# Optimization experiments

Measured on AMD Instinct MI355X. Metric: run time of the kernel, lower is better.

## Reference

```python
import jax, jax.numpy as jnp
import numpy as np

WINDOW = 21
PATCH = 1
H_PARAM = 0.1
EPS = 1e-10


def _box_sum(x, w):
    # Sum over a w x w sliding window (VALID), per (batch, channel).
    return jax.lax.reduce_window(x, 0.0, jax.lax.add,
                                 (1, 1, w, w), (1, 1, 1, 1), 'VALID')


def setup_inputs() -> dict:
    key = jax.random.key(0)
    noisy = jax.random.uniform(key, (8, 3, 512, 512), dtype=jnp.float32)
    return {"noisy": noisy}


def reference(noisy) -> jnp.ndarray:
    # Faithful vectorization of the per-pixel loop for patch_size=1.
    # For each pixel p=(i,j):
    #   window = padded[i:i+W, j:j+W]; center = noisy[i,j]
    #   dists  = mean((window - center)^2)
    #   weights = exp(-dists / h^2)            # shape (B, C)
    #   patch  = window[0, 0] = padded[i, j]   # top-left of window (half_patch=0)
    #   out[:, c, i, j] = sum_b weights[b,c] * patch[b,c]   (sum over BATCH)
    #   wsum[:, c, i, j] = sum_b weights[b,c]
    # out = clamp(out / (wsum + 1e-10), 0, 1)
    h2 = H_PARAM * H_PARAM
    W = WINDOW
    pad = W // 2
    B, C, Hh, Ww = noisy.shape
    padded = jnp.pad(noisy, ((0, 0), (0, 0), (pad, pad), (pad, pad)), mode='reflect')

    # mean((window - center)^2) = (S2 - 2*center*S1 + W^2*center^2) / W^2
    s1 = _box_sum(padded, W)                  # (B, C, H, W)
    s2 = _box_sum(padded * padded, W)
    n_win = jnp.asarray(W * W, dtype=noisy.dtype)
    dists = (s2 - 2.0 * noisy * s1 + n_win * noisy * noisy) / n_win

    weights = jnp.exp(-dists / h2)            # (B, C, H, W)
    patch = padded[:, :, :Hh, :Ww]            # top-left pixel of each window

    num = jnp.sum(weights * patch, axis=0, keepdims=True)   # (1, C, H, W)
    den = jnp.sum(weights, axis=0, keepdims=True)
    out = num / (den + EPS)
    out = jnp.broadcast_to(out, noisy.shape)  # loop assigns same row to all b
    return jnp.clip(out, 0.0, 1.0)
```

## Files before the change

### kernel.cpp

```cpp
#include <hip/hip_runtime.h>

#define B 8
#define CCH 3
#define HH 512
#define WW 512
#define WIN 21
#define PAD 10
#define TSX 32
#define TSY 32
#define PTY 52
#define TROW 60
#define HSH 53
#define NSLOT 676

__global__ __launch_bounds__(256, 3) void nlm_fused_kernel(const float* __restrict__ noisy,
                                                           float* __restrict__ out) {
    __shared__ float  tile[PTY][TROW];
    __shared__ float2 hs_t[TSX][HSH];

    const int tid = threadIdx.x;
    const int x0 = blockIdx.x * TSX;
    const int y0 = blockIdx.y * TSY;
    const int ch = blockIdx.z;

    int   rowbase[3], gxs[3];
    float* ldsp[3];
    bool  valid[3], edge[3];
    #pragma unroll
    for (int k = 0; k < 3; ++k) {
        int s = tid + 256 * k;
        valid[k] = (s < NSLOT);
        int ss = valid[k] ? s : 0;
        int r  = ss / 13;
        int c4 = ss - r * 13;
        int gy = y0 + r - PAD;
        gy = (gy < 0) ? -gy : ((gy >= HH) ? (2 * (HH - 1) - gy) : gy);
        int gx = x0 + (c4 << 2) - PAD;
        rowbase[k] = gy * WW;
        gxs[k]     = gx;
        edge[k]    = (gx < 0) || (gx > WW - 4);
        ldsp[k]    = &tile[r][c4 << 2];
    }

    const float* src0 = noisy + (size_t)ch * (HH * WW);
    float4 pre[3];
    #pragma unroll
    for (int k = 0; k < 3; ++k) {
        if (valid[k]) {
            if (!edge[k]) {
                pre[k] = *(const float4*)(src0 + rowbase[k] + gxs[k]);
            } else {
                float tmp[4];
                #pragma unroll
                for (int t = 0; t < 4; ++t) {
                    int gx = gxs[k] + t;
                    gx = (gx < 0) ? -gx : ((gx >= WW) ? (2 * (WW - 1) - gx) : gx);
                    tmp[t] = src0[rowbase[k] + gx];
                }
                pre[k] = make_float4(tmp[0], tmp[1], tmp[2], tmp[3]);
            }
        }
    }

    float num[4] = {0.f, 0.f, 0.f, 0.f};
    float den[4] = {0.f, 0.f, 0.f, 0.f};

    const int tx  = tid & 31;
    const int ty0 = (tid >> 5) << 2;

    for (int b = 0; b < B; ++b) {
        __syncthreads();
        #pragma unroll
        for (int k = 0; k < 3; ++k)
            if (valid[k]) *(float4*)ldsp[k] = pre[k];
        __syncthreads();

        if (b < B - 1) {
            const float* srcn = noisy + (size_t)((b + 1) * CCH + ch) * (HH * WW);
            #pragma unroll
            for (int k = 0; k < 3; ++k) {
                if (valid[k]) {
                    if (!edge[k]) {
                        pre[k] = *(const float4*)(srcn + rowbase[k] + gxs[k]);
                    } else {
                        float tmp[4];
                        #pragma unroll
                        for (int t = 0; t < 4; ++t) {
                            int gx = gxs[k] + t;
                            gx = (gx < 0) ? -gx : ((gx >= WW) ? (2 * (WW - 1) - gx) : gx);
                            tmp[t] = srcn[rowbase[k] + gx];
                        }
                        pre[k] = make_float4(tmp[0], tmp[1], tmp[2], tmp[3]);
                    }
                }
            }
        }

        if (tid < PTY * 4) {
            int r   = tid >> 2;
            int cx0 = (tid & 3) << 3;
            float v[28];
            #pragma unroll
            for (int q = 0; q < 7; ++q)
                *(float4*)&v[q * 4] = *(const float4*)&tile[r][cx0 + (q << 2)];
            float s1 = 0.f, s2 = 0.f;
            #pragma unroll
            for (int k = 0; k <= 20; ++k) { s1 += v[k]; s2 = fmaf(v[k], v[k], s2); }
            hs_t[cx0][r] = make_float2(s1, s2);
            #pragma unroll
            for (int j = 1; j < 8; ++j) {
                float vo = v[j - 1], vn = v[j + 20];
                s1 += vn - vo;
                s2 += vn * vn - vo * vo;
                hs_t[cx0 + j][r] = make_float2(s1, s2);
            }
        }
        __syncthreads();

        float2 h0 = hs_t[tx][ty0];
        float2 h1 = hs_t[tx][ty0 + 1];
        float2 h2 = hs_t[tx][ty0 + 2];
        float vs1 = h0.x + h1.x + h2.x;
        float vs2 = h0.y + h1.y + h2.y;
        #pragma unroll
        for (int k = 3; k <= 20; ++k) {
            float2 h = hs_t[tx][ty0 + k];
            vs1 += h.x;
            vs2 += h.y;
        }
        const float kE = (-100.0f / 441.0f) * 1.44269504088896f;
        {
            float a = tile[ty0 + PAD][tx + PAD];
            float p = tile[ty0][tx];
            float dd = fmaf(a, fmaf(441.f, a, -2.f * vs1), vs2);
            float w = exp2f(dd * kE);
            num[0] += w * p; den[0] += w;
        }
        #pragma unroll
        for (int i = 1; i < 4; ++i) {
            float2 hn = hs_t[tx][ty0 + 20 + i];
            float2 ho = (i == 1) ? h0 : ((i == 2) ? h1 : h2);
            vs1 += hn.x - ho.x;
            vs2 += hn.y - ho.y;
            float a = tile[ty0 + i + PAD][tx + PAD];
            float p = tile[ty0 + i][tx];
            float dd = fmaf(a, fmaf(441.f, a, -2.f * vs1), vs2);
            float w = exp2f(dd * kE);
            num[i] += w * p; den[i] += w;
        }
    }

    #pragma unroll
    for (int i = 0; i < 4; ++i) {
        int y = y0 + ty0 + i;
        int x = x0 + tx;
        float v = num[i] / (den[i] + 1e-10f);
        v = v < 0.f ? 0.f : (v > 1.f ? 1.f : v);
        #pragma unroll
        for (int b = 0; b < B; ++b)
            out[((size_t)(b * CCH + ch) * HH + y) * WW + x] = v;
    }
}

extern "C" void kernel_launch(void* const* d_in, const int* in_sizes, int n_in,
                              void* d_out, int out_size, void* d_ws, size_t ws_size,
                              hipStream_t stream) {
    const float* noisy = (const float*)d_in[0];
    float* out = (float*)d_out;
    dim3 grid(WW / TSX, HH / TSY, CCH);
    nlm_fused_kernel<<<grid, dim3(256), 0, stream>>>(noisy, out);
}
```

Baseline: 88.96 us.

## Drop shared input tile; load horizontal sums directly from global with double-buffered LDS

Removes the shared-memory input tile and its staging stores. Each horizontal-sum thread now reads its 32-wide row segment straight from global memory, and each output thread loads its center and patch pixels directly. The horizontal-sum buffer is double-buffered, so each batch iteration needs only one barrier instead of three. The cost is more redundant global/L2 traffic, since overlapping halo reads are no longer shared and the register prefetch of the next batch is gone, which could expose load latency.

```diff
diff --git a/kernel.cpp b/kernel.cpp
--- a/kernel.cpp
+++ b/kernel.cpp
@@ -4,161 +4,124 @@
 #define CCH 3
 #define HH 512
 #define WW 512
+#define HW (HH * WW)
 #define WIN 21
 #define PAD 10
 #define TSX 32
 #define TSY 32
-#define PTY 52
-#define TROW 60
+#define ROWS 52
 #define HSH 53
-#define NSLOT 676
 
 __global__ __launch_bounds__(256, 3) void nlm_fused_kernel(const float* __restrict__ noisy,
                                                            float* __restrict__ out) {
-    __shared__ float  tile[PTY][TROW];
-    __shared__ float2 hs_t[TSX][HSH];
+    __shared__ float2 hs[2][TSX][HSH];
 
     const int tid = threadIdx.x;
     const int x0 = blockIdx.x * TSX;
     const int y0 = blockIdx.y * TSY;
     const int ch = blockIdx.z;
 
-    int   rowbase[3], gxs[3];
-    float* ldsp[3];
-    bool  valid[3], edge[3];
+    const int hr   = tid >> 2;
+    const int hsg  = tid & 3;
+    const bool hact = (tid < ROWS * 4);
+    int gy = y0 + hr - PAD;
+    gy = (gy < 0) ? -gy : ((gy >= HH) ? (2 * (HH - 1) - gy) : gy);
+    const int hrow = gy * WW;
+    const int xb   = x0 + (hsg << 3) - 12;
+    const bool hedge = (xb < 0) || (xb + 31 > WW - 1);
+
+    const int tx  = tid & 31;
+    const int ty0 = (tid >> 5) << 2;
+    int aoff[4], poff[4];
+    int pc = x0 + tx - PAD;
+    pc = (pc < 0) ? -pc : pc;
     #pragma unroll
-    for (int k = 0; k < 3; ++k) {
-        int s = tid + 256 * k;
-        valid[k] = (s < NSLOT);
-        int ss = valid[k] ? s : 0;
-        int r  = ss / 13;
-        int c4 = ss - r * 13;
-        int gy = y0 + r - PAD;
-        gy = (gy < 0) ? -gy : ((gy >= HH) ? (2 * (HH - 1) - gy) : gy);
-        int gx = x0 + (c4 << 2) - PAD;
-        rowbase[k] = gy * WW;
-        gxs[k]     = gx;
-        edge[k]    = (gx < 0) || (gx > WW - 4);
-        ldsp[k]    = &tile[r][c4 << 2];
-    }
-
-    const float* src0 = noisy + (size_t)ch * (HH * WW);
-    float4 pre[3];
-    #pragma unroll
-    for (int k = 0; k < 3; ++k) {
-        if (valid[k]) {
-            if (!edge[k]) {
-                pre[k] = *(const float4*)(src0 + rowbase[k] + gxs[k]);
-            } else {
-                float tmp[4];
-                #pragma unroll
-                for (int t = 0; t < 4; ++t) {
-                    int gx = gxs[k] + t;
-                    gx = (gx < 0) ? -gx : ((gx >= WW) ? (2 * (WW - 1) - gx) : gx);
-                    tmp[t] = src0[rowbase[k] + gx];
-                }
-                pre[k] = make_float4(tmp[0], tmp[1], tmp[2], tmp[3]);
-            }
-        }
+    for (int i = 0; i < 4; ++i) {
+        const int ay = y0 + ty0 + i;
+        aoff[i] = ay * WW + (x0 + tx);
+        int py = ay - PAD;
+        py = (py < 0) ? -py : py;
+        poff[i] = py * WW + pc;
     }
 
     float num[4] = {0.f, 0.f, 0.f, 0.f};
     float den[4] = {0.f, 0.f, 0.f, 0.f};
+    const float kE = (-100.0f / 441.0f) * 1.44269504088896f;
 
-    const int tx  = tid & 31;
-    const int ty0 = (tid >> 5) << 2;
+    int cur = 0;
+    for (int b = 0; b < B; ++b) {
+        const float* src = noisy + (size_t)(b * CCH + ch) * HW;
 
-    for (int b = 0; b < B; ++b) {
-        __syncthreads();
+        float a[4], p[4];
         #pragma unroll
-        for (int k = 0; k < 3; ++k)
-            if (valid[k]) *(float4*)ldsp[k] = pre[k];
-        __syncthreads();
+        for (int i = 0; i < 4; ++i) { a[i] = src[aoff[i]]; p[i] = src[poff[i]]; }
 
-        if (b < B - 1) {
-            const float* srcn = noisy + (size_t)((b + 1) * CCH + ch) * (HH * WW);
-            #pragma unroll
-            for (int k = 0; k < 3; ++k) {
-                if (valid[k]) {
-                    if (!edge[k]) {
-                        pre[k] = *(const float4*)(srcn + rowbase[k] + gxs[k]);
-                    } else {
-                        float tmp[4];
-                        #pragma unroll
-                        for (int t = 0; t < 4; ++t) {
-                            int gx = gxs[k] + t;
-                            gx = (gx < 0) ? -gx : ((gx >= WW) ? (2 * (WW - 1) - gx) : gx);
-                            tmp[t] = srcn[rowbase[k] + gx];
-                        }
-                        pre[k] = make_float4(tmp[0], tmp[1], tmp[2], tmp[3]);
-                    }
+        if (hact) {
+            float w[32];
+            if (!hedge) {
+                #pragma unroll
+                for (int q = 0; q < 8; ++q)
+                    *(float4*)&w[q * 4] = *(const float4*)(src + hrow + xb + (q << 2));
+            } else {
+                #pragma unroll
+                for (int m = 0; m < 28; ++m) {
+                    int gx = xb + 2 + m;
+                    gx = (gx < 0) ? -gx : ((gx >= WW) ? (2 * (WW - 1) - gx) : gx);
+                    w[m + 2] = src[hrow + gx];
                 }
             }
-        }
-
-        if (tid < PTY * 4) {
-            int r   = tid >> 2;
-            int cx0 = (tid & 3) << 3;
-            float v[28];
-            #pragma unroll
-            for (int q = 0; q < 7; ++q)
-                *(float4*)&v[q * 4] = *(const float4*)&tile[r][cx0 + (q << 2)];
             float s1 = 0.f, s2 = 0.f;
             #pragma unroll
-            for (int k = 0; k <= 20; ++k) { s1 += v[k]; s2 = fmaf(v[k], v[k], s2); }
-            hs_t[cx0][r] = make_float2(s1, s2);
+            for (int k = 0; k < 21; ++k) { s1 += w[k + 2]; s2 = fmaf(w[k + 2], w[k + 2], s2); }
+            const int c0 = hsg << 3;
+            hs[cur][c0][hr] = make_float2(s1, s2);
             #pragma unroll
             for (int j = 1; j < 8; ++j) {
-                float vo = v[j - 1], vn = v[j + 20];
+                float vo = w[j + 1], vn = w[j + 22];
                 s1 += vn - vo;
                 s2 += vn * vn - vo * vo;
-                hs_t[cx0 + j][r] = make_float2(s1, s2);
+                hs[cur][c0 + j][hr] = make_float2(s1, s2);
             }
         }
         __syncthreads();
 
-        float2 h0 = hs_t[tx][ty0];
-        float2 h1 = hs_t[tx][ty0 + 1];
-        float2 h2 = hs_t[tx][ty0 + 2];
+        const float2* col = &hs[cur][tx][0];
+        float2 h0 = col[ty0], h1 = col[ty0 + 1], h2 = col[ty0 + 2];
         float vs1 = h0.x + h1.x + h2.x;
         float vs2 = h0.y + h1.y + h2.y;
         #pragma unroll
         for (int k = 3; k <= 20; ++k) {
-            float2 h = hs_t[tx][ty0 + k];
+            float2 h = col[ty0 + k];
             vs1 += h.x;
             vs2 += h.y;
         }
-        const float kE = (-100.0f / 441.0f) * 1.44269504088896f;
         {
-            float a = tile[ty0 + PAD][tx + PAD];
-            float p = tile[ty0][tx];
-            float dd = fmaf(a, fmaf(441.f, a, -2.f * vs1), vs2);
-            float w = exp2f(dd * kE);
-            num[0] += w * p; den[0] += w;
+            float dd = fmaf(a[0], fmaf(441.f, a[0], -2.f * vs1), vs2);
+            float wgt = exp2f(dd * kE);
+            num[0] = fmaf(wgt, p[0], num[0]); den[0] += wgt;
         }
         #pragma unroll
         for (int i = 1; i < 4; ++i) {
-            float2 hn = hs_t[tx][ty0 + 20 + i];
+            float2 hn = col[ty0 + 20 + i];
             float2 ho = (i == 1) ? h0 : ((i == 2) ? h1 : h2);
             vs1 += hn.x - ho.x;
             vs2 += hn.y - ho.y;
-            float a = tile[ty0 + i + PAD][tx + PAD];
-            float p = tile[ty0 + i][tx];
-            float dd = fmaf(a, fmaf(441.f, a, -2.f * vs1), vs2);
-            float w = exp2f(dd * kE);
-            num[i] += w * p; den[i] += w;
+            float dd = fmaf(a[i], fmaf(441.f, a[i], -2.f * vs1), vs2);
+            float wgt = exp2f(dd * kE);
+            num[i] = fmaf(wgt, p[i], num[i]); den[i] += wgt;
         }
+        cur ^= 1;
     }
 
     #pragma unroll
     for (int i = 0; i < 4; ++i) {
-        int y = y0 + ty0 + i;
-        int x = x0 + tx;
+        const int y = y0 + ty0 + i;
+        const int x = x0 + tx;
         float v = num[i] / (den[i] + 1e-10f);
         v = v < 0.f ? 0.f : (v > 1.f ? 1.f : v);
         #pragma unroll
-        for (int b = 0; b < B; ++b)
-            out[((size_t)(b * CCH + ch) * HH + y) * WW + x] = v;
+        for (int bb = 0; bb < B; ++bb)
+            out[((size_t)(bb * CCH + ch) * HH + y) * WW + x] = v;
     }
 }
 
```

Result: slower. 138.2 us (+55.4%).

## Halve tile height to 16 rows and double-buffer the LDS tile

Applied to the files above, without the earlier changes.

Shrinks each block to a 32x16 output tile with 128 threads, doubling the grid to give more blocks for latency hiding, at the cost of a larger halo fraction (36 loaded rows for 16 output rows instead of 52 for 32). The shared tile becomes double-buffered so one of the two per-batch barriers can be dropped. Each thread now does up to two horizontal-sum tasks. The extra halo means more redundant global loads and horizontal-sum work per output pixel.

```diff
diff --git a/kernel.cpp b/kernel.cpp
--- a/kernel.cpp
+++ b/kernel.cpp
@@ -7,15 +7,17 @@
 #define WIN 21
 #define PAD 10
 #define TSX 32
-#define TSY 32
-#define PTY 52
+#define TSY 16
+#define PTY 36
 #define TROW 60
-#define HSH 53
-#define NSLOT 676
+#define HSH 37
+#define NSLOT 468
+#define NTHR 128
+#define HTASK (PTY * 4)
 
-__global__ __launch_bounds__(256, 3) void nlm_fused_kernel(const float* __restrict__ noisy,
-                                                           float* __restrict__ out) {
-    __shared__ float  tile[PTY][TROW];
+__global__ __launch_bounds__(NTHR, 3) void nlm_fused_kernel(const float* __restrict__ noisy,
+                                                            float* __restrict__ out) {
+    __shared__ float  tile[2][PTY][TROW];
     __shared__ float2 hs_t[TSX][HSH];
 
     const int tid = threadIdx.x;
@@ -23,12 +25,12 @@
     const int y0 = blockIdx.y * TSY;
     const int ch = blockIdx.z;
 
-    int   rowbase[3], gxs[3];
-    float* ldsp[3];
-    bool  valid[3], edge[3];
+    int   rowbase[4], gxs[4];
+    float* ldsp[4];
+    bool  valid[4], edge[4];
     #pragma unroll
-    for (int k = 0; k < 3; ++k) {
-        int s = tid + 256 * k;
+    for (int k = 0; k < 4; ++k) {
+        int s = tid + NTHR * k;
         valid[k] = (s < NSLOT);
         int ss = valid[k] ? s : 0;
         int r  = ss / 13;
@@ -39,13 +41,13 @@
         rowbase[k] = gy * WW;
         gxs[k]     = gx;
         edge[k]    = (gx < 0) || (gx > WW - 4);
-        ldsp[k]    = &tile[r][c4 << 2];
+        ldsp[k]    = &tile[0][r][c4 << 2];
     }
 
     const float* src0 = noisy + (size_t)ch * (HH * WW);
-    float4 pre[3];
+    float4 pre[4];
     #pragma unroll
-    for (int k = 0; k < 3; ++k) {
+    for (int k = 0; k < 4; ++k) {
         if (valid[k]) {
             if (!edge[k]) {
                 pre[k] = *(const float4*)(src0 + rowbase[k] + gxs[k]);
@@ -67,18 +69,19 @@
 
     const int tx  = tid & 31;
     const int ty0 = (tid >> 5) << 2;
+    const float kE = (-100.0f / 441.0f) * 1.44269504088896f;
 
+    int par = 0;
     for (int b = 0; b < B; ++b) {
-        __syncthreads();
         #pragma unroll
-        for (int k = 0; k < 3; ++k)
-            if (valid[k]) *(float4*)ldsp[k] = pre[k];
+        for (int k = 0; k < 4; ++k)
+            if (valid[k]) *(float4*)(ldsp[k] + par * (PTY * TROW)) = pre[k];
         __syncthreads();
 
         if (b < B - 1) {
             const float* srcn = noisy + (size_t)((b + 1) * CCH + ch) * (HH * WW);
             #pragma unroll
-            for (int k = 0; k < 3; ++k) {
+            for (int k = 0; k < 4; ++k) {
                 if (valid[k]) {
                     if (!edge[k]) {
                         pre[k] = *(const float4*)(srcn + rowbase[k] + gxs[k]);
@@ -96,13 +99,13 @@
             }
         }
 
-        if (tid < PTY * 4) {
-            int r   = tid >> 2;
-            int cx0 = (tid & 3) << 3;
+        auto hwork = [&](int t) {
+            int r   = t >> 2;
+            int cx0 = (t & 3) << 3;
             float v[28];
             #pragma unroll
             for (int q = 0; q < 7; ++q)
-                *(float4*)&v[q * 4] = *(const float4*)&tile[r][cx0 + (q << 2)];
+                *(float4*)&v[q * 4] = *(const float4*)&tile[par][r][cx0 + (q << 2)];
             float s1 = 0.f, s2 = 0.f;
             #pragma unroll
             for (int k = 0; k <= 20; ++k) { s1 += v[k]; s2 = fmaf(v[k], v[k], s2); }
@@ -114,7 +117,9 @@
                 s2 += vn * vn - vo * vo;
                 hs_t[cx0 + j][r] = make_float2(s1, s2);
             }
-        }
+        };
+        hwork(tid);
+        if (tid < HTASK - NTHR) hwork(tid + NTHR);
         __syncthreads();
 
         float2 h0 = hs_t[tx][ty0];
@@ -128,10 +133,9 @@
             vs1 += h.x;
             vs2 += h.y;
         }
-        const float kE = (-100.0f / 441.0f) * 1.44269504088896f;
         {
-            float a = tile[ty0 + PAD][tx + PAD];
-            float p = tile[ty0][tx];
+            float a = tile[par][ty0 + PAD][tx + PAD];
+            float p = tile[par][ty0][tx];
             float dd = fmaf(a, fmaf(441.f, a, -2.f * vs1), vs2);
             float w = exp2f(dd * kE);
             num[0] += w * p; den[0] += w;
@@ -142,12 +146,13 @@
             float2 ho = (i == 1) ? h0 : ((i == 2) ? h1 : h2);
             vs1 += hn.x - ho.x;
             vs2 += hn.y - ho.y;
-            float a = tile[ty0 + i + PAD][tx + PAD];
-            float p = tile[ty0 + i][tx];
+            float a = tile[par][ty0 + i + PAD][tx + PAD];
+            float p = tile[par][ty0 + i][tx];
             float dd = fmaf(a, fmaf(441.f, a, -2.f * vs1), vs2);
             float w = exp2f(dd * kE);
             num[i] += w * p; den[i] += w;
         }
+        par ^= 1;
     }
 
     #pragma unroll
@@ -157,8 +162,8 @@
         float v = num[i] / (den[i] + 1e-10f);
         v = v < 0.f ? 0.f : (v > 1.f ? 1.f : v);
         #pragma unroll
-        for (int b = 0; b < B; ++b)
-            out[((size_t)(b * CCH + ch) * HH + y) * WW + x] = v;
+        for (int bb = 0; bb < B; ++bb)
+            out[((size_t)(bb * CCH + ch) * HH + y) * WW + x] = v;
     }
 }
 
@@ -168,5 +173,5 @@
     const float* noisy = (const float*)d_in[0];
     float* out = (float*)d_out;
     dim3 grid(WW / TSX, HH / TSY, CCH);
-    nlm_fused_kernel<<<grid, dim3(256), 0, stream>>>(noisy, out);
+    nlm_fused_kernel<<<grid, dim3(NTHR), 0, stream>>>(noisy, out);
 }
```

Result: slower. 99.40 us (+11.7%).

## Double-buffer LDS tiles and use a lightweight LDS-only barrier

Applied to the files above, without the earlier changes.

The shared tile and horizontal-sum buffers are duplicated and alternate by batch parity. This removes the leading __syncthreads that kept the next batch's store from racing with reads of the previous one. The remaining barriers become an inline s_waitcnt lgkmcnt(0) plus s_barrier. That barrier does not wait on outstanding global loads, so the prefetch of the next batch can stay in flight across it. The cost is roughly double the LDS per block, which at 3 blocks per CU sits close to the per-CU LDS limit and could reduce occupancy.

```diff
diff --git a/kernel.cpp b/kernel.cpp
--- a/kernel.cpp
+++ b/kernel.cpp
@@ -13,10 +13,16 @@
 #define HSH 53
 #define NSLOT 676
 
+__device__ __forceinline__ void lds_barrier() {
+    asm volatile("s_waitcnt lgkmcnt(0)" ::: "memory");
+    __builtin_amdgcn_s_barrier();
+    asm volatile("" ::: "memory");
+}
+
 __global__ __launch_bounds__(256, 3) void nlm_fused_kernel(const float* __restrict__ noisy,
                                                            float* __restrict__ out) {
-    __shared__ float  tile[PTY][TROW];
-    __shared__ float2 hs_t[TSX][HSH];
+    __shared__ float  tile[2][PTY][TROW];
+    __shared__ float2 hs_t[2][TSX][HSH];
 
     const int tid = threadIdx.x;
     const int x0 = blockIdx.x * TSX;
@@ -39,7 +45,7 @@
         rowbase[k] = gy * WW;
         gxs[k]     = gx;
         edge[k]    = (gx < 0) || (gx > WW - 4);
-        ldsp[k]    = &tile[r][c4 << 2];
+        ldsp[k]    = &tile[0][r][c4 << 2];
     }
 
     const float* src0 = noisy + (size_t)ch * (HH * WW);
@@ -67,13 +73,14 @@
 
     const int tx  = tid & 31;
     const int ty0 = (tid >> 5) << 2;
+    const float kE = (-100.0f / 441.0f) * 1.44269504088896f;
 
+    int par = 0;
     for (int b = 0; b < B; ++b) {
-        __syncthreads();
         #pragma unroll
         for (int k = 0; k < 3; ++k)
-            if (valid[k]) *(float4*)ldsp[k] = pre[k];
-        __syncthreads();
+            if (valid[k]) *(float4*)(ldsp[k] + par * (PTY * TROW)) = pre[k];
+        lds_barrier();
 
         if (b < B - 1) {
             const float* srcn = noisy + (size_t)((b + 1) * CCH + ch) * (HH * WW);
@@ -102,52 +109,52 @@
             float v[28];
             #pragma unroll
             for (int q = 0; q < 7; ++q)
-                *(float4*)&v[q * 4] = *(const float4*)&tile[r][cx0 + (q << 2)];
+                *(float4*)&v[q * 4] = *(const float4*)&tile[par][r][cx0 + (q << 2)];
             float s1 = 0.f, s2 = 0.f;
             #pragma unroll
             for (int k = 0; k <= 20; ++k) { s1 += v[k]; s2 = fmaf(v[k], v[k], s2); }
-            hs_t[cx0][r] = make_float2(s1, s2);
+            hs_t[par][cx0][r] = make_float2(s1, s2);
             #pragma unroll
             for (int j = 1; j < 8; ++j) {
                 float vo = v[j - 1], vn = v[j + 20];
                 s1 += vn - vo;
                 s2 += vn * vn - vo * vo;
-                hs_t[cx0 + j][r] = make_float2(s1, s2);
+                hs_t[par][cx0 + j][r] = make_float2(s1, s2);
             }
         }
-        __syncthreads();
+        lds_barrier();
 
-        float2 h0 = hs_t[tx][ty0];
-        float2 h1 = hs_t[tx][ty0 + 1];
-        float2 h2 = hs_t[tx][ty0 + 2];
+        float2 h0 = hs_t[par][tx][ty0];
+        float2 h1 = hs_t[par][tx][ty0 + 1];
+        float2 h2 = hs_t[par][tx][ty0 + 2];
         float vs1 = h0.x + h1.x + h2.x;
         float vs2 = h0.y + h1.y + h2.y;
         #pragma unroll
         for (int k = 3; k <= 20; ++k) {
-            float2 h = hs_t[tx][ty0 + k];
+            float2 h = hs_t[par][tx][ty0 + k];
             vs1 += h.x;
             vs2 += h.y;
         }
-        const float kE = (-100.0f / 441.0f) * 1.44269504088896f;
         {
-            float a = tile[ty0 + PAD][tx + PAD];
-            float p = tile[ty0][tx];
+            float a = tile[par][ty0 + PAD][tx + PAD];
+            float p = tile[par][ty0][tx];
             float dd = fmaf(a, fmaf(441.f, a, -2.f * vs1), vs2);
             float w = exp2f(dd * kE);
             num[0] += w * p; den[0] += w;
         }
         #pragma unroll
         for (int i = 1; i < 4; ++i) {
-            float2 hn = hs_t[tx][ty0 + 20 + i];
+            float2 hn = hs_t[par][tx][ty0 + 20 + i];
             float2 ho = (i == 1) ? h0 : ((i == 2) ? h1 : h2);
             vs1 += hn.x - ho.x;
             vs2 += hn.y - ho.y;
-            float a = tile[ty0 + i + PAD][tx + PAD];
-            float p = tile[ty0 + i][tx];
+            float a = tile[par][ty0 + i + PAD][tx + PAD];
+            float p = tile[par][ty0 + i][tx];
             float dd = fmaf(a, fmaf(441.f, a, -2.f * vs1), vs2);
             float w = exp2f(dd * kE);
             num[i] += w * p; den[i] += w;
         }
+        par ^= 1;
     }
 
     #pragma unroll
```

New measurement: 89.09 us. No clear change (+0.1%).
